# Optimization experiments

Measured on AMD Instinct MI355X. Metric: run time of the kernel, lower is better.

## Reference

```python
import jax, jax.numpy as jnp
import numpy as np
from jax.scipy.linalg import expm

NUM_WIRES = 10
DIM = 2 ** NUM_WIRES  # 1024, statevector dimension
N_GATES = 8


def setup_inputs() -> dict:
    key = jax.random.key(0)
    kf, kg, kt = jax.random.split(key, 3)
    # feature to be amplitude-embedded (AmplitudeEmbedding pads with 0 and L2-normalizes)
    feature = jax.random.normal(kf, (DIM,), jnp.float32)
    # dense Hermitian gate generators (real symmetric), one per selected gate
    A = jax.random.normal(kg, (N_GATES, DIM, DIM), jnp.float32) / np.float32(np.sqrt(DIM))
    gens = 0.5 * (A + jnp.swapaxes(A, -1, -2))
    # learned parameters theta, shape (n_gates, 1) as in the flax module
    theta = jax.random.normal(kt, (N_GATES, 1), jnp.float32)
    return {"feature": feature, "theta": theta, "gens": gens}


def reference(feature, theta, gens):
    # AmplitudeEmbedding: pad (no-op here, len == DIM) then L2-normalize -> complex state
    psi = (feature / jnp.linalg.norm(feature)).astype(jnp.complex64)  # [DIM]

    def apply_gate(psi, gate):
        G, t = gate  # G: [DIM, DIM] complex, t: scalar complex
        U = expm(-1j * t * G)          # qml.exp(-1j * theta * gen)
        return U @ psi, None

    gens_c = gens.astype(jnp.complex64)
    thetas_c = theta[:, 0].astype(jnp.complex64)
    psi, _ = jax.lax.scan(apply_gate, psi, (gens_c, thetas_c))
    # qml.probs(wires=all): Born-rule probabilities over the full register
    return jnp.real(psi * jnp.conj(psi)).astype(jnp.float32)  # [DIM]
```

## Files before the change

### kernel.cpp

```cpp
#include <hip/hip_runtime.h>

#define DIM   1024
#define NG    8
#define NBLK  128
#define TPB   512
#define WAVES (TPB / 64)
#define ROWS_PER_BLK WAVES
#define SCALE    1.45f
#define INVSCALE (1.0f / SCALE)
#define CTOL  5e-3f
#define KMAX  12
#define FSTRIDE 16

typedef unsigned long long u64;
union f2u { float2 f; u64 u; };


__global__ __launch_bounds__(TPB) void qsim_kernel(
    const float* __restrict__ feat,
    const float* __restrict__ theta,
    const float* __restrict__ gens,
    float*       __restrict__ out,
    u64*         __restrict__ vbuf0,
    u64*         __restrict__ vbuf1,
    unsigned*    __restrict__ flags)
{
  const int tid  = threadIdx.x;
  const int lane = tid & 63;
  const int wid  = tid >> 6;
  const int bid  = blockIdx.x;
  const int row  = bid * ROWS_PER_BLK + wid;

  __shared__ float2   smemV[DIM];
  __shared__ float    red[WAVES];
  __shared__ unsigned wdone;
  __shared__ unsigned ready;

  float a[16];
  {
    const float* Gr = gens + (size_t)row * DIM;
    #pragma unroll
    for (int p = 0; p < 16; ++p) a[p] = Gr[p * 64 + lane];
  }

  if (tid == 0) { wdone = 0; ready = 0; }
  {
    float f0 = feat[tid], f1 = feat[tid + TPB];
    float s = f0 * f0 + f1 * f1;
    #pragma unroll
    for (int mm = 1; mm < 64; mm <<= 1) s += __shfl_xor(s, mm);
    if (lane == 0) red[wid] = s;
  }
  __syncthreads();
  float tot = 0.f;
  #pragma unroll
  for (int i = 0; i < WAVES; ++i) tot += red[i];
  const float inv = 1.0f / sqrtf(tot);

  float pr = feat[row] * inv;
  float pi = 0.f;

  unsigned pub = 0;
  bool pendG = false;

  auto publish = [&](float sr, float si) {
    u64* dst = ((pub + 1) & 1) ? vbuf1 : vbuf0;
    if (lane == 0) {
      f2u x; x.f = make_float2(sr, si);
      __hip_atomic_store(dst + row, x.u,
                         __ATOMIC_RELAXED, __HIP_MEMORY_SCOPE_AGENT);
    }
    __builtin_amdgcn_sched_barrier(0);
    __builtin_amdgcn_s_waitcnt(0);
    __builtin_amdgcn_sched_barrier(0);
    ++pub;
    if (lane == 0) {
      unsigned old = atomicAdd(&wdone, 1u);
      if (old == WAVES * pub - 1) {
        __hip_atomic_store(flags + bid * FSTRIDE, pub,
                           __ATOMIC_RELAXED, __HIP_MEMORY_SCOPE_AGENT);
      }
    }
  };

  auto wait_all = [&]() {
    if (wid == 0) {
      unsigned a0 = __hip_atomic_load(flags + lane * FSTRIDE,
                                      __ATOMIC_RELAXED, __HIP_MEMORY_SCOPE_AGENT);
      unsigned b0 = __hip_atomic_load(flags + (lane + 64) * FSTRIDE,
                                      __ATOMIC_RELAXED, __HIP_MEMORY_SCOPE_AGENT);
      unsigned a1 = __hip_atomic_load(flags + lane * FSTRIDE,
                                      __ATOMIC_RELAXED, __HIP_MEMORY_SCOPE_AGENT);
      unsigned b1 = __hip_atomic_load(flags + (lane + 64) * FSTRIDE,
                                      __ATOMIC_RELAXED, __HIP_MEMORY_SCOPE_AGENT);
      unsigned a2 = __hip_atomic_load(flags + lane * FSTRIDE,
                                      __ATOMIC_RELAXED, __HIP_MEMORY_SCOPE_AGENT);
      unsigned b2 = __hip_atomic_load(flags + (lane + 64) * FSTRIDE,
                                      __ATOMIC_RELAXED, __HIP_MEMORY_SCOPE_AGENT);
      unsigned a3 = __hip_atomic_load(flags + lane * FSTRIDE,
                                      __ATOMIC_RELAXED, __HIP_MEMORY_SCOPE_AGENT);
      unsigned b3 = __hip_atomic_load(flags + (lane + 64) * FSTRIDE,
                                      __ATOMIC_RELAXED, __HIP_MEMORY_SCOPE_AGENT);
      for (;;) {
        if (__all((((int)(a0 - pub) >= 0) & ((int)(b0 - pub) >= 0)))) break;
        __builtin_amdgcn_s_sleep(1);
        a0 = a1; b0 = b1; a1 = a2; b1 = b2; a2 = a3; b2 = b3;
        a3 = __hip_atomic_load(flags + lane * FSTRIDE,
                               __ATOMIC_RELAXED, __HIP_MEMORY_SCOPE_AGENT);
        b3 = __hip_atomic_load(flags + (lane + 64) * FSTRIDE,
                               __ATOMIC_RELAXED, __HIP_MEMORY_SCOPE_AGENT);
      }
      if (lane == 0)
        __hip_atomic_store(&ready, pub, __ATOMIC_RELAXED,
                           __HIP_MEMORY_SCOPE_WORKGROUP);
    } else {
      while ((int)(__hip_atomic_load(&ready, __ATOMIC_RELAXED,
                                     __HIP_MEMORY_SCOPE_WORKGROUP) - pub) < 0) {
        __builtin_amdgcn_s_sleep(1);
      }
    }
  };

  for (int g = 0; g < NG; ++g) {
    const float  th = theta[g];
    const double z  = (double)th * (double)SCALE;
    const double az = fmax(fabs(z), 1e-6);
    const float  sg = (th < 0.f) ? -1.f : 1.f;

    double bv[19];
    bv[18] = 1e-30;
    bv[17] = (36.0 / az) * 1e-30;
    #pragma unroll
    for (int k = 17; k >= 1; --k)
      bv[k - 1] = (2.0 * (double)k / az) * bv[k] - bv[k + 1];
    double S = bv[0];
    #pragma unroll
    for (int k = 2; k <= 18; k += 2) S += 2.0 * bv[k];
    const double invS = 1.0 / S;

    float jc[KMAX + 2];
    #pragma unroll
    for (int k = 0; k <= KMAX + 1; ++k) jc[k] = (float)(bv[k] * invS);

    int m = KMAX; bool found = false;
    #pragma unroll
    for (int k = 1; k <= KMAX; ++k) {
      if (!found && (double)(k + 1) > az &&
          fabs(bv[k + 1] * invS) < (double)CTOL) { m = k; found = true; }
    }

    float accr = jc[0] * pr, acci = jc[0] * pi;
    float wm1r = pr, wm1i = pi, wm2r = 0.f, wm2i = 0.f;

    #pragma unroll
    for (int k = 1; k <= KMAX; ++k) {
      if (k > m) break;

      float2 v[16];
      if (g == 0 && k == 1) {
        #pragma unroll
        for (int p = 0; p < 16; ++p)
          v[p] = make_float2(feat[p * 64 + lane] * inv, 0.f);
      } else {
        wait_all();
        const u64* vsrc = (pub & 1) ? vbuf1 : vbuf0;
        f2u x0, x1;
        x0.u = __hip_atomic_load(vsrc + wid * 128 + lane,
                                 __ATOMIC_RELAXED, __HIP_MEMORY_SCOPE_AGENT);
        x1.u = __hip_atomic_load(vsrc + wid * 128 + 64 + lane,
                                 __ATOMIC_RELAXED, __HIP_MEMORY_SCOPE_AGENT);
        __builtin_amdgcn_sched_barrier(0);
        if (pendG) {
          const float* Gr = gens + (size_t)g * DIM * DIM + (size_t)row * DIM;
          #pragma unroll
          for (int p = 0; p < 16; ++p) a[p] = Gr[p * 64 + lane];
          pendG = false;
        }
        __builtin_amdgcn_sched_barrier(0);
        smemV[wid * 128 + lane]      = x0.f;
        smemV[wid * 128 + 64 + lane] = x1.f;
        __syncthreads();
        #pragma unroll
        for (int p = 0; p < 16; ++p) v[p] = smemV[p * 64 + lane];
      }

      float yr = 0.f, yi = 0.f;
      #pragma unroll
      for (int p = 0; p < 16; ++p) {
        yr = fmaf(a[p], v[p].x, yr);
        yi = fmaf(a[p], v[p].y, yi);
      }
      #pragma unroll
      for (int mm = 1; mm < 64; mm <<= 1) {
        yr += __shfl_xor(yr, mm);
        yi += __shfl_xor(yi, mm);
      }

      const float ur = yr * INVSCALE;
      const float ui = yi * INVSCALE;
      const float wkr = (k == 1) ? ur : fmaf(2.f, ur, -wm2r);
      const float wki = (k == 1) ? ui : fmaf(2.f, ui, -wm2i);

      const bool last = (k == m);
      if (!last) publish(wkr, wki);

      {
        const float j2  = 2.f * jc[k];
        const float sj2 = sg * j2;
        if ((k & 3) == 0) {
          accr = fmaf(j2, wkr, accr);
          acci = fmaf(j2, wki, acci);
        } else if ((k & 3) == 1) {
          accr = fmaf( sj2, wki, accr);
          acci = fmaf(-sj2, wkr, acci);
        } else if ((k & 3) == 2) {
          accr = fmaf(-j2, wkr, accr);
          acci = fmaf(-j2, wki, acci);
        } else {
          accr = fmaf(-sj2, wki, accr);
          acci = fmaf( sj2, wkr, acci);
        }
      }

      if (last) {
        if (g < NG - 1) {
          publish(accr, acci);
          if (wid != 0) {
            const float* Gr = gens + (size_t)(g + 1) * DIM * DIM
                                   + (size_t)row * DIM;
            #pragma unroll
            for (int p = 0; p < 16; ++p) a[p] = Gr[p * 64 + lane];
          } else {
            pendG = true;
          }
        }
      } else {
        wm2r = wm1r; wm2i = wm1i;
        wm1r = wkr;  wm1i = wki;
      }
    }
    pr = accr; pi = acci;
  }

  if (lane == 0) out[row] = pr * pr + pi * pi;
}

extern "C" void kernel_launch(void* const* d_in, const int* in_sizes, int n_in,
                              void* d_out, int out_size, void* d_ws, size_t ws_size,
                              hipStream_t stream) {
  const float* feat  = (const float*)d_in[0];
  const float* theta = (const float*)d_in[1];
  const float* gens  = (const float*)d_in[2];
  float* out = (float*)d_out;

  unsigned* flags = (unsigned*)d_ws;
  u64* vbuf0 = (u64*)((char*)d_ws + 8192);
  u64* vbuf1 = (u64*)((char*)d_ws + 8192 + (size_t)DIM * sizeof(u64));

  qsim_kernel<<<dim3(NBLK), dim3(TPB), 0, stream>>>(
      feat, theta, gens, out, vbuf0, vbuf1, flags);
}
```

Measured before the change: 154.4 us.

## Let wave 0 gather the vector for the block and prefetch next gate rows

Wave 0 now polls the grid flags, loads the entire published vector from global memory into LDS and releases a workgroup-scope ready flag. The other waves acquire that flag and read the vector from LDS, so the per-step __syncthreads and the split per-wave global loads are gone. The next gate's generator rows are prefetched into a separate register array after the first Chebyshev step instead of being loaded at the end of the gate. This costs 16 extra registers per thread, and the s_waitcnt(0) in the following publish may now also wait on those prefetch loads.

```diff
diff --git a/kernel.cpp b/kernel.cpp
--- a/kernel.cpp
+++ b/kernel.cpp
@@ -61,15 +61,16 @@
   float pi = 0.f;
 
   unsigned pub = 0;
-  bool pendG = false;
-
-  auto publish = [&](float sr, float si) {
+
+  auto pub_store = [&](float sr, float si) {
     u64* dst = ((pub + 1) & 1) ? vbuf1 : vbuf0;
     if (lane == 0) {
       f2u x; x.f = make_float2(sr, si);
       __hip_atomic_store(dst + row, x.u,
                          __ATOMIC_RELAXED, __HIP_MEMORY_SCOPE_AGENT);
     }
+  };
+  auto pub_commit = [&]() {
     __builtin_amdgcn_sched_barrier(0);
     __builtin_amdgcn_s_waitcnt(0);
     __builtin_amdgcn_sched_barrier(0);
@@ -83,44 +84,6 @@
     }
   };
 
-  auto wait_all = [&]() {
-    if (wid == 0) {
-      unsigned a0 = __hip_atomic_load(flags + lane * FSTRIDE,
-                                      __ATOMIC_RELAXED, __HIP_MEMORY_SCOPE_AGENT);
-      unsigned b0 = __hip_atomic_load(flags + (lane + 64) * FSTRIDE,
-                                      __ATOMIC_RELAXED, __HIP_MEMORY_SCOPE_AGENT);
-      unsigned a1 = __hip_atomic_load(flags + lane * FSTRIDE,
-                                      __ATOMIC_RELAXED, __HIP_MEMORY_SCOPE_AGENT);
-      unsigned b1 = __hip_atomic_load(flags + (lane + 64) * FSTRIDE,
-                                      __ATOMIC_RELAXED, __HIP_MEMORY_SCOPE_AGENT);
-      unsigned a2 = __hip_atomic_load(flags + lane * FSTRIDE,
-                                      __ATOMIC_RELAXED, __HIP_MEMORY_SCOPE_AGENT);
-      unsigned b2 = __hip_atomic_load(flags + (lane + 64) * FSTRIDE,
-                                      __ATOMIC_RELAXED, __HIP_MEMORY_SCOPE_AGENT);
-      unsigned a3 = __hip_atomic_load(flags + lane * FSTRIDE,
-                                      __ATOMIC_RELAXED, __HIP_MEMORY_SCOPE_AGENT);
-      unsigned b3 = __hip_atomic_load(flags + (lane + 64) * FSTRIDE,
-                                      __ATOMIC_RELAXED, __HIP_MEMORY_SCOPE_AGENT);
-      for (;;) {
-        if (__all((((int)(a0 - pub) >= 0) & ((int)(b0 - pub) >= 0)))) break;
-        __builtin_amdgcn_s_sleep(1);
-        a0 = a1; b0 = b1; a1 = a2; b1 = b2; a2 = a3; b2 = b3;
-        a3 = __hip_atomic_load(flags + lane * FSTRIDE,
-                               __ATOMIC_RELAXED, __HIP_MEMORY_SCOPE_AGENT);
-        b3 = __hip_atomic_load(flags + (lane + 64) * FSTRIDE,
-                               __ATOMIC_RELAXED, __HIP_MEMORY_SCOPE_AGENT);
-      }
-      if (lane == 0)
-        __hip_atomic_store(&ready, pub, __ATOMIC_RELAXED,
-                           __HIP_MEMORY_SCOPE_WORKGROUP);
-    } else {
-      while ((int)(__hip_atomic_load(&ready, __ATOMIC_RELAXED,
-                                     __HIP_MEMORY_SCOPE_WORKGROUP) - pub) < 0) {
-        __builtin_amdgcn_s_sleep(1);
-      }
-    }
-  };
-
   for (int g = 0; g < NG; ++g) {
     const float  th = theta[g];
     const double z  = (double)th * (double)SCALE;
@@ -151,6 +114,7 @@
 
     float accr = jc[0] * pr, acci = jc[0] * pi;
     float wm1r = pr, wm1i = pi, wm2r = 0.f, wm2i = 0.f;
+    float anext[16];
 
     #pragma unroll
     for (int k = 1; k <= KMAX; ++k) {
@@ -162,26 +126,52 @@
         for (int p = 0; p < 16; ++p)
           v[p] = make_float2(feat[p * 64 + lane] * inv, 0.f);
       } else {
-        wait_all();
-        const u64* vsrc = (pub & 1) ? vbuf1 : vbuf0;
-        f2u x0, x1;
-        x0.u = __hip_atomic_load(vsrc + wid * 128 + lane,
-                                 __ATOMIC_RELAXED, __HIP_MEMORY_SCOPE_AGENT);
-        x1.u = __hip_atomic_load(vsrc + wid * 128 + 64 + lane,
-                                 __ATOMIC_RELAXED, __HIP_MEMORY_SCOPE_AGENT);
-        __builtin_amdgcn_sched_barrier(0);
-        if (pendG) {
-          const float* Gr = gens + (size_t)g * DIM * DIM + (size_t)row * DIM;
-          #pragma unroll
-          for (int p = 0; p < 16; ++p) a[p] = Gr[p * 64 + lane];
-          pendG = false;
+        if (wid == 0) {
+          unsigned a0 = __hip_atomic_load(flags + lane * FSTRIDE,
+                                          __ATOMIC_RELAXED, __HIP_MEMORY_SCOPE_AGENT);
+          unsigned b0 = __hip_atomic_load(flags + (lane + 64) * FSTRIDE,
+                                          __ATOMIC_RELAXED, __HIP_MEMORY_SCOPE_AGENT);
+          unsigned a1 = __hip_atomic_load(flags + lane * FSTRIDE,
+                                          __ATOMIC_RELAXED, __HIP_MEMORY_SCOPE_AGENT);
+          unsigned b1 = __hip_atomic_load(flags + (lane + 64) * FSTRIDE,
+                                          __ATOMIC_RELAXED, __HIP_MEMORY_SCOPE_AGENT);
+          unsigned a2 = __hip_atomic_load(flags + lane * FSTRIDE,
+                                          __ATOMIC_RELAXED, __HIP_MEMORY_SCOPE_AGENT);
+          unsigned b2 = __hip_atomic_load(flags + (lane + 64) * FSTRIDE,
+                                          __ATOMIC_RELAXED, __HIP_MEMORY_SCOPE_AGENT);
+          unsigned a3 = __hip_atomic_load(flags + lane * FSTRIDE,
+                                          __ATOMIC_RELAXED, __HIP_MEMORY_SCOPE_AGENT);
+          unsigned b3 = __hip_atomic_load(flags + (lane + 64) * FSTRIDE,
+                                          __ATOMIC_RELAXED, __HIP_MEMORY_SCOPE_AGENT);
+          for (;;) {
+            if (__all((((int)(a0 - pub) >= 0) & ((int)(b0 - pub) >= 0)))) break;
+            __builtin_amdgcn_s_sleep(1);
+            a0 = a1; b0 = b1; a1 = a2; b1 = b2; a2 = a3; b2 = b3;
+            a3 = __hip_atomic_load(flags + lane * FSTRIDE,
+                                   __ATOMIC_RELAXED, __HIP_MEMORY_SCOPE_AGENT);
+            b3 = __hip_atomic_load(flags + (lane + 64) * FSTRIDE,
+                                   __ATOMIC_RELAXED, __HIP_MEMORY_SCOPE_AGENT);
+          }
+          const u64* vsrc = (pub & 1) ? vbuf1 : vbuf0;
+          f2u x[16];
+          #pragma unroll
+          for (int p = 0; p < 16; ++p)
+            x[p].u = __hip_atomic_load(vsrc + p * 64 + lane,
+                                       __ATOMIC_RELAXED, __HIP_MEMORY_SCOPE_AGENT);
+          #pragma unroll
+          for (int p = 0; p < 16; ++p) smemV[p * 64 + lane] = x[p].f;
+          __hip_atomic_store(&ready, pub, __ATOMIC_RELEASE,
+                             __HIP_MEMORY_SCOPE_WORKGROUP);
+          #pragma unroll
+          for (int p = 0; p < 16; ++p) v[p] = x[p].f;
+        } else {
+          while ((int)(__hip_atomic_load(&ready, __ATOMIC_ACQUIRE,
+                                         __HIP_MEMORY_SCOPE_WORKGROUP) - pub) < 0) {
+            __builtin_amdgcn_s_sleep(1);
+          }
+          #pragma unroll
+          for (int p = 0; p < 16; ++p) v[p] = smemV[p * 64 + lane];
         }
-        __builtin_amdgcn_sched_barrier(0);
-        smemV[wid * 128 + lane]      = x0.f;
-        smemV[wid * 128 + 64 + lane] = x1.f;
-        __syncthreads();
-        #pragma unroll
-        for (int p = 0; p < 16; ++p) v[p] = smemV[p * 64 + lane];
       }
 
       float yr = 0.f, yi = 0.f;
@@ -202,7 +192,7 @@
       const float wki = (k == 1) ? ui : fmaf(2.f, ui, -wm2i);
 
       const bool last = (k == m);
-      if (!last) publish(wkr, wki);
+      if (!last) pub_store(wkr, wki);
 
       {
         const float j2  = 2.f * jc[k];
@@ -222,22 +212,29 @@
         }
       }
 
+      if (!last) pub_commit();
+
+      if (k == 1 && g < NG - 1) {
+        const float* Gr = gens + (size_t)(g + 1) * DIM * DIM
+                               + (size_t)row * DIM;
+        #pragma unroll
+        for (int p = 0; p < 16; ++p) anext[p] = Gr[p * 64 + lane];
+      }
+
       if (last) {
         if (g < NG - 1) {
-          publish(accr, acci);
-          if (wid != 0) {
-            const float* Gr = gens + (size_t)(g + 1) * DIM * DIM
-                                   + (size_t)row * DIM;
-            #pragma unroll
-            for (int p = 0; p < 16; ++p) a[p] = Gr[p * 64 + lane];
-          } else {
-            pendG = true;
-          }
+          pub_store(accr, acci);
+          pub_commit();
         }
       } else {
         wm2r = wm1r; wm2i = wm1i;
         wm1r = wkr;  wm1i = wki;
       }
+    }
+
+    if (g < NG - 1) {
+      #pragma unroll
+      for (int p = 0; p < 16; ++p) a[p] = anext[p];
     }
     pr = accr; pi = acci;
   }
```

Result: no change. 155.5 us (+0.7%).
